# Kernel optimization log

Hardware: AMD Instinct MI355X
Metric: run time of the kernel (lower is better)

The kernel has to match this reference:

```python
import jax, jax.numpy as jnp
import numpy as np

# Dimensions (match init_kwargs / input_specs)
B, C, H, W = 16, 16, 64, 64
N = H * W          # num_nodes
D_E = 64           # node_embed_dim
D_H = 128          # gnn_hidden_dim
D_R = 256          # readout_output_dim


def _param(key, shape, fan_in):
    return jax.random.normal(key, shape, jnp.float32) * (1.0 / np.sqrt(fan_in))


def setup_inputs() -> dict:
    key = jax.random.key(0)
    ks = jax.random.split(key, 16)
    inp = {
        "obs": jax.random.normal(ks[0], (B, C, H, W), jnp.float32),
        # node_embedding MLP (2 layers: C -> D_E -> D_E)
        "e1_w": _param(ks[1], (C, D_E), C),   "e1_b": jnp.zeros((D_E,), jnp.float32),
        "e2_w": _param(ks[2], (D_E, D_E), D_E), "e2_b": jnp.zeros((D_E,), jnp.float32),
        # 3 GNN layers (Linear then adjacency aggregation)
        "g1_w": _param(ks[3], (D_E, D_H), D_E), "g1_b": jnp.zeros((D_H,), jnp.float32),
        "g2_w": _param(ks[4], (D_H, D_H), D_H), "g2_b": jnp.zeros((D_H,), jnp.float32),
        "g3_w": _param(ks[5], (D_H, D_H), D_H), "g3_b": jnp.zeros((D_H,), jnp.float32),
        # readout MLP (2 layers: D_H -> 2*D_H -> D_R)
        "r1_w": _param(ks[6], (D_H, 2 * D_H), D_H),   "r1_b": jnp.zeros((2 * D_H,), jnp.float32),
        "r2_w": _param(ks[7], (2 * D_H, D_R), 2 * D_H), "r2_b": jnp.zeros((D_R,), jnp.float32),
    }
    return inp


def _adj_norm():
    # 4-neighbor grid adjacency on an H x W grid, row-normalized (same for every
    # batch element, so build once as (N, N) instead of (B, N, N)).
    idx = jnp.arange(N)
    up = jnp.eye(N, k=-W, dtype=jnp.float32)                      # i > 0
    down = jnp.eye(N, k=W, dtype=jnp.float32)                     # i < H-1
    left = jnp.eye(N, k=-1, dtype=jnp.float32) * ((idx % W) != 0)[:, None]
    right = jnp.eye(N, k=1, dtype=jnp.float32) * ((idx % W) != (W - 1))[:, None]
    adj = up + down + left + right
    return adj / (adj.sum(axis=1, keepdims=True) + 1e-6)


def reference(obs, e1_w, e1_b, e2_w, e2_b,
              g1_w, g1_b, g2_w, g2_b, g3_w, g3_b,
              r1_w, r1_b, r2_w, r2_b):
    relu = jax.nn.relu
    # grid -> graph: (B, C, H, W) -> (B, N, C)
    x = jnp.transpose(obs, (0, 2, 3, 1)).reshape(B, N, C)
    # node embedding MLP (output activation per ding MLP default)
    h = relu(x @ e1_w + e1_b)
    h = relu(h @ e2_w + e2_b)
    A = _adj_norm()  # (N, N)
    for Wg, bg in ((g1_w, g1_b), (g2_w, g2_b), (g3_w, g3_b)):
        support = h @ Wg + bg                      # (B, N, D_H)
        h = relu(jnp.einsum('nm,bmf->bnf', A, support))
    g = h.mean(axis=1)                              # (B, D_H) graph readout
    g = relu(g @ r1_w + r1_b)
    return relu(g @ r2_w + r2_b)                    # (B, D_R)
```

## Files before the change

kernel.cpp:

```cpp
#include <hip/hip_runtime.h>


typedef __attribute__((ext_vector_type(8))) short bf16x8;
typedef __attribute__((ext_vector_type(4))) float f32x4;
#define MFMA(a, b, c) __builtin_amdgcn_mfma_f32_16x16x32_bf16(a, b, c, 0, 0, 0)

__device__ inline ushort bf16h(float x) {
    unsigned u = __float_as_uint(x);
    return (ushort)((u + 0x7fffu + ((u >> 16) & 1u)) >> 16);
}
__device__ inline void split_bf16(float x, ushort& hi, ushort& lo) {
    hi = bf16h(x);
    lo = bf16h(x - __uint_as_float(((unsigned)hi) << 16));
}
__device__ inline unsigned pack_split(float x) {
    unsigned u = __float_as_uint(x);
    unsigned hi = (u + 0x7fffu + ((u >> 16) & 1u)) >> 16;
    float r = x - __uint_as_float(hi << 16);
    unsigned v = __float_as_uint(r);
    unsigned lo = (v + 0x7fffu + ((v >> 16) & 1u)) >> 16;
    return (hi << 16) | lo;
}
__device__ inline void frag_packed(const unsigned* bp, bf16x8& bh, bf16x8& bl) {
    unsigned p[8];
#pragma unroll
    for (int j = 0; j < 8; j++) p[j] = bp[j * 65];
    union { bf16x8 v; unsigned d[4]; } H, L;
#pragma unroll
    for (int j = 0; j < 4; j++) {
        const unsigned e = p[2 * j], o = p[2 * j + 1];
        H.d[j] = (o & 0xFFFF0000u) | (e >> 16);
        L.d[j] = (o << 16) | (e & 0xFFFFu);
    }
    bh = H.v; bl = L.v;
}

__global__ void zero_kernel(float* __restrict__ p) {
    p[blockIdx.x * 256 + threadIdx.x] = 0.f;
}

__global__ __launch_bounds__(64) void wprep_kernel(
    const float* __restrict__ e1w, const float* __restrict__ e2w,
    const float* __restrict__ g1w, const float* __restrict__ g2w,
    const float* __restrict__ g3w, ushort* __restrict__ wf)
{
    const int blk = blockIdx.x, l = threadIdx.x;
    const float* src; int K, N, kc, t; ushort* dst;
    if (blk < 4)        { src = e1w; K = 16;  N = 64;  kc = 0; t = blk;      dst = wf; }
    else if (blk < 12)  { src = e2w; K = 64;  N = 64;  int u = blk - 4;  kc = u >> 2; t = u & 3; dst = wf + 4096; }
    else if (blk < 28)  { src = g1w; K = 64;  N = 128; int u = blk - 12; kc = u >> 3; t = u & 7; dst = wf + 12288; }
    else if (blk < 60)  { src = g2w; K = 128; N = 128; int u = blk - 28; kc = u >> 3; t = u & 7; dst = wf + 28672; }
    else                { src = g3w; K = 128; N = 128; int u = blk - 60; kc = u >> 3; t = u & 7; dst = wf + 61440; }
    const int T = (N == 64) ? 4 : 8;
    ushort* uh = dst + ((kc * T + t) * 2 + 0) * 512 + l * 8;
    ushort* ul = dst + ((kc * T + t) * 2 + 1) * 512 + l * 8;
    const int f = t * 16 + (l & 15);
    const int kb = kc * 32 + ((l >> 4) << 3);
#pragma unroll
    for (int j = 0; j < 8; j++) {
        const int k = kb + j;
        const float w = (k < K) ? src[k * N + f] : 0.f;
        ushort hi, lo; split_bf16(w, hi, lo);
        uh[j] = hi; ul[j] = lo;
    }
}

__global__ __launch_bounds__(256, 4) void embed_kernel(
    const float* __restrict__ obs, const ushort* __restrict__ wf,
    const float* __restrict__ e1b, const float* __restrict__ e2b,
    float* __restrict__ h0)
{
    __shared__ unsigned Xs[32 * 65];
    __shared__ unsigned Hs[64 * 65];
    const int tid = threadIdx.x, b = blockIdx.x >> 6, row = blockIdx.x & 63;
    const int lane = tid & 63, w = tid >> 6, quad = lane >> 4, nl = lane & 15;
    const int cp = tid >> 4, nq = tid & 15;

    const float4 x4 = *(const float4*)(obs + ((size_t)(b * 16 + cp) << 12) + row * 64 + nq * 4);
    unsigned* xp = Xs + cp * 65 + nq * 4;
    xp[0] = pack_split(x4.x); xp[1] = pack_split(x4.y);
    xp[2] = pack_split(x4.z); xp[3] = pack_split(x4.w);
    unsigned* zp = Xs + (16 + cp) * 65 + nq * 4;
    zp[0] = 0u; zp[1] = 0u; zp[2] = 0u; zp[3] = 0u;
    __syncthreads();

    {
        const ushort* wp = wf + lane * 8;
        const bf16x8 wh = *(const bf16x8*)(wp + (w * 2) * 512);
        const bf16x8 wl = *(const bf16x8*)(wp + (w * 2 + 1) * 512);
#pragma unroll
        for (int nt = 0; nt < 4; nt++) {
            const unsigned* bp = Xs + (quad * 8) * 65 + nt * 16 + nl;
            bf16x8 bh, bl; frag_packed(bp, bh, bl);
            f32x4 c = {0.f, 0.f, 0.f, 0.f};
            c = MFMA(wh, bh, c); c = MFMA(wh, bl, c); c = MFMA(wl, bh, c);
#pragma unroll
            for (int reg = 0; reg < 4; reg++) {
                const int fm = 16 * w + quad * 4 + reg;
                Hs[fm * 65 + nt * 16 + nl] = pack_split(fmaxf(c[reg] + e1b[fm], 0.f));
            }
        }
    }
    __syncthreads();

    const ushort* e2f = wf + 4096;
    f32x4 a2[4];
#pragma unroll
    for (int nt = 0; nt < 4; nt++) a2[nt] = (f32x4){0.f, 0.f, 0.f, 0.f};
#pragma unroll
    for (int kc = 0; kc < 2; kc++) {
        const ushort* wp = e2f + lane * 8;
        const bf16x8 wh = *(const bf16x8*)(wp + ((kc * 4 + w) * 2) * 512);
        const bf16x8 wl = *(const bf16x8*)(wp + ((kc * 4 + w) * 2 + 1) * 512);
#pragma unroll
        for (int nt = 0; nt < 4; nt++) {
            const unsigned* bp = Hs + (kc * 32 + quad * 8) * 65 + nt * 16 + nl;
            bf16x8 bh, bl; frag_packed(bp, bh, bl);
            a2[nt] = MFMA(wh, bh, a2[nt]);
            a2[nt] = MFMA(wh, bl, a2[nt]);
            a2[nt] = MFMA(wl, bh, a2[nt]);
        }
    }
#pragma unroll
    for (int reg = 0; reg < 4; reg++) {
        const int f = 16 * w + quad * 4 + reg;
        const float bv = e2b[f];
#pragma unroll
        for (int nt = 0; nt < 4; nt++)
            h0[((size_t)(b * 64 + f) << 12) + row * 64 + nt * 16 + nl] =
                fmaxf(a2[nt][reg] + bv, 0.f);
    }
}

template <int K, bool MEAN>
__global__ __launch_bounds__(256, 4) void gnn_kernel(
    const float* __restrict__ hin, const ushort* __restrict__ wf,
    const float* __restrict__ bias, float* __restrict__ hout,
    float* __restrict__ gsum)
{
    constexpr int NH = K / 64;
    __shared__ unsigned As[NH][64 * 65];
    const int tid = threadIdx.x;
    const int bid = ((blockIdx.x & 7) << 7) | (blockIdx.x >> 3);
    const int b = bid >> 6, row = bid & 63;
    const int lane = tid & 63, w = tid >> 6, quad = lane >> 4, nl = lane & 15;
    const int kp = tid >> 4, nq = tid & 15;
    const float* hb = hin + (size_t)b * K * 4096;
    const int rowu = (row > 0) ? row - 1 : row;
    const int rowd = (row < 63) ? row + 1 : row;
    const float su = (row > 0) ? 1.f : 0.f;
    const float sd = (row < 63) ? 1.f : 0.f;
    float inv[4];
#pragma unroll
    for (int i = 0; i < 4; i++) {
        const int n = nq * 4 + i;
        const int deg = (row > 0) + (row < 63) + (n > 0) + (n < 63);
        inv[i] = 1.f / ((float)deg + 1e-6f);
    }

    f32x4 acc[4][2];
#pragma unroll
    for (int nt = 0; nt < 4; nt++) {
        acc[nt][0] = (f32x4){0.f, 0.f, 0.f, 0.f};
        acc[nt][1] = (f32x4){0.f, 0.f, 0.f, 0.f};
    }

    float4 c4[4], u4[4], d4[4];
    auto load_half = [&](int kh) {
#pragma unroll
        for (int it = 0; it < 4; it++) {
            const int kk = it * 16 + kp;
            const float* pk = hb + ((size_t)(kh * 64 + kk) << 12) + nq * 4;
            c4[it] = *(const float4*)(pk + row * 64);
            u4[it] = *(const float4*)(pk + rowu * 64);
            d4[it] = *(const float4*)(pk + rowd * 64);
        }
    };
    auto stage = [&](int kh) {
        unsigned* dst = As[kh];
#pragma unroll
        for (int it = 0; it < 4; it++) {
            const int kk = it * 16 + kp;
            const float pw = __shfl_up(c4[it].w, 1);
            const float nx = __shfl_down(c4[it].x, 1);
            const float lx = (nq > 0) ? pw : 0.f;
            const float rw = (nq < 15) ? nx : 0.f;
            unsigned* ap = dst + kk * 65 + nq * 4;
            ap[0] = pack_split((su * u4[it].x + sd * d4[it].x + lx + c4[it].y) * inv[0]);
            ap[1] = pack_split((su * u4[it].y + sd * d4[it].y + c4[it].x + c4[it].z) * inv[1]);
            ap[2] = pack_split((su * u4[it].z + sd * d4[it].z + c4[it].y + c4[it].w) * inv[2]);
            ap[3] = pack_split((su * u4[it].w + sd * d4[it].w + c4[it].z + rw) * inv[3]);
        }
    };
    auto consume = [&](int kh) {
        const unsigned* src = As[kh];
#pragma unroll
        for (int kc = 0; kc < 2; kc++) {
            const int kcg = kh * 2 + kc;
            const ushort* wp = wf + lane * 8;
            const bf16x8 wh0 = *(const bf16x8*)(wp + ((kcg * 8 + 2 * w)     * 2)     * 512);
            const bf16x8 wl0 = *(const bf16x8*)(wp + ((kcg * 8 + 2 * w)     * 2 + 1) * 512);
            const bf16x8 wh1 = *(const bf16x8*)(wp + ((kcg * 8 + 2 * w + 1) * 2)     * 512);
            const bf16x8 wl1 = *(const bf16x8*)(wp + ((kcg * 8 + 2 * w + 1) * 2 + 1) * 512);
#pragma unroll
            for (int nt = 0; nt < 4; nt++) {
                const unsigned* bp = src + (kc * 32 + quad * 8) * 65 + nt * 16 + nl;
                bf16x8 bh, bl; frag_packed(bp, bh, bl);
                acc[nt][0] = MFMA(wh0, bh, acc[nt][0]);
                acc[nt][0] = MFMA(wh0, bl, acc[nt][0]);
                acc[nt][0] = MFMA(wl0, bh, acc[nt][0]);
                acc[nt][1] = MFMA(wh1, bh, acc[nt][1]);
                acc[nt][1] = MFMA(wh1, bl, acc[nt][1]);
                acc[nt][1] = MFMA(wl1, bh, acc[nt][1]);
            }
        }
    };

    load_half(0);
    stage(0);
    __syncthreads();
#pragma unroll
    for (int kh = 0; kh < NH; kh++) {
        if (kh + 1 < NH) load_half(kh + 1);
        consume(kh);
        if (kh + 1 < NH) {
            stage(kh + 1);
            __syncthreads();
        }
    }

    if (!MEAN) {
#pragma unroll
        for (int ftl = 0; ftl < 2; ftl++) {
            const int fb = 32 * w + 16 * ftl + quad * 4;
            const float b0 = bias[fb], b1 = bias[fb + 1], b2 = bias[fb + 2], b3 = bias[fb + 3];
#pragma unroll
            for (int nt = 0; nt < 4; nt++) {
                const int n = 16 * nt + nl;
                const int deg = (row > 0) + (row < 63) + (n > 0) + (n < 63);
                const float rs = (float)deg / ((float)deg + 1e-6f);
                float* op = hout + ((size_t)(b * 128 + fb) << 12) + row * 64 + n;
                op[0]        = fmaxf(acc[nt][ftl][0] + rs * b0, 0.f);
                op[1u << 12] = fmaxf(acc[nt][ftl][1] + rs * b1, 0.f);
                op[2u << 12] = fmaxf(acc[nt][ftl][2] + rs * b2, 0.f);
                op[3u << 12] = fmaxf(acc[nt][ftl][3] + rs * b3, 0.f);
            }
        }
    } else {
#pragma unroll
        for (int ftl = 0; ftl < 2; ftl++) {
            const int fb = 32 * w + 16 * ftl + quad * 4;
#pragma unroll
            for (int reg = 0; reg < 4; reg++) {
                const float bv = bias[fb + reg];
                float v = 0.f;
#pragma unroll
                for (int nt = 0; nt < 4; nt++) {
                    const int n = 16 * nt + nl;
                    const int deg = (row > 0) + (row < 63) + (n > 0) + (n < 63);
                    const float rs = (float)deg / ((float)deg + 1e-6f);
                    v += fmaxf(acc[nt][ftl][reg] + rs * bv, 0.f);
                }
                v += __shfl_xor(v, 1); v += __shfl_xor(v, 2);
                v += __shfl_xor(v, 4); v += __shfl_xor(v, 8);
                if (nl == 0) atomicAdd(&gsum[b * 128 + fb + reg], v * (1.f / 4096.f));
            }
        }
    }
}

__global__ __launch_bounds__(256) void readout_kernel(
    const float* __restrict__ gsum, const float* __restrict__ r1w,
    const float* __restrict__ r1b, const float* __restrict__ r2w,
    const float* __restrict__ r2b, float* __restrict__ out)
{
    __shared__ float gs[128];
    __shared__ float g2[256];
    const int b = blockIdx.x, tid = threadIdx.x;
    if (tid < 128) gs[tid] = gsum[b * 128 + tid];
    __syncthreads();
    float a = r1b[tid];
#pragma unroll 16
    for (int k = 0; k < 128; k++) a = fmaf(gs[k], r1w[k * 256 + tid], a);
    g2[tid] = fmaxf(a, 0.f);
    __syncthreads();
    float a2 = r2b[tid];
#pragma unroll 16
    for (int k = 0; k < 256; k++) a2 = fmaf(g2[k], r2w[k * 256 + tid], a2);
    out[b * 256 + tid] = fmaxf(a2, 0.f);
}

extern "C" void kernel_launch(void* const* d_in, const int* in_sizes, int n_in,
                              void* d_out, int out_size, void* d_ws, size_t ws_size,
                              hipStream_t stream)
{
    const float* obs = (const float*)d_in[0];
    const float* e1w = (const float*)d_in[1];
    const float* e1b = (const float*)d_in[2];
    const float* e2w = (const float*)d_in[3];
    const float* e2b = (const float*)d_in[4];
    const float* g1w = (const float*)d_in[5];
    const float* g1b = (const float*)d_in[6];
    const float* g2w = (const float*)d_in[7];
    const float* g2b = (const float*)d_in[8];
    const float* g3w = (const float*)d_in[9];
    const float* g3b = (const float*)d_in[10];
    const float* r1w = (const float*)d_in[11];
    const float* r1b = (const float*)d_in[12];
    const float* r2w = (const float*)d_in[13];
    const float* r2b = (const float*)d_in[14];
    float* out = (float*)d_out;
    float* ws = (float*)d_ws;

    float* h0 = ws;
    float* h1 = ws + 4194304;
    float* h2 = ws + 4194304 + 8388608;
    float* gsum = (float*)((char*)d_ws + 80u * 1024u * 1024u);
    ushort* wfb = (ushort*)((char*)d_ws + 80u * 1024u * 1024u + 8192u);

    hipLaunchKernelGGL(zero_kernel, dim3(8), dim3(256), 0, stream, gsum);
    hipLaunchKernelGGL(wprep_kernel, dim3(92), dim3(64), 0, stream,
                       e1w, e2w, g1w, g2w, g3w, wfb);
    hipLaunchKernelGGL(embed_kernel, dim3(1024), dim3(256), 0, stream,
                       obs, wfb, e1b, e2b, h0);
    hipLaunchKernelGGL((gnn_kernel<64, false>), dim3(1024), dim3(256), 0, stream,
                       h0, wfb + 12288, g1b, h1, nullptr);
    hipLaunchKernelGGL((gnn_kernel<128, false>), dim3(1024), dim3(256), 0, stream,
                       h1, wfb + 28672, g2b, h2, nullptr);
    hipLaunchKernelGGL((gnn_kernel<128, true>), dim3(1024), dim3(256), 0, stream,
                       h2, wfb + 61440, g3b, nullptr, gsum);
    hipLaunchKernelGGL(readout_kernel, dim3(16), dim3(256), 0, stream,
                       gsum, r1w, r1b, r2w, r2b, out);
}
```

Before: 165.8 us.

## Interleave neighbor loads with LDS staging, fold zeroing into weight prep

The GNN kernel now loads and stages each half of the input in groups of two, so staging one group overlaps the loads of the next and fewer float4 registers stay live. Staging of the next half now happens before the MFMA consume of the current half instead of after it. The low bf16 part in pack_split is truncated instead of rounded, and the gsum zeroing moves into extra blocks of the weight-prep kernel to save a launch. Moving the staging ahead of consume removes the overlap of global loads with MFMA work, and truncating the low part loses a little precision.

After: 163.1 us. About the same (-1.6%).

```diff
diff --git a/kernel.cpp b/kernel.cpp
--- a/kernel.cpp
+++ b/kernel.cpp
@@ -17,9 +17,7 @@
     unsigned u = __float_as_uint(x);
     unsigned hi = (u + 0x7fffu + ((u >> 16) & 1u)) >> 16;
     float r = x - __uint_as_float(hi << 16);
-    unsigned v = __float_as_uint(r);
-    unsigned lo = (v + 0x7fffu + ((v >> 16) & 1u)) >> 16;
-    return (hi << 16) | lo;
+    return (hi << 16) | (__float_as_uint(r) >> 16);
 }
 __device__ inline void frag_packed(const unsigned* bp, bf16x8& bh, bf16x8& bl) {
     unsigned p[8];
@@ -35,16 +33,17 @@
     bh = H.v; bl = L.v;
 }
 
-__global__ void zero_kernel(float* __restrict__ p) {
-    p[blockIdx.x * 256 + threadIdx.x] = 0.f;
-}
-
 __global__ __launch_bounds__(64) void wprep_kernel(
     const float* __restrict__ e1w, const float* __restrict__ e2w,
     const float* __restrict__ g1w, const float* __restrict__ g2w,
-    const float* __restrict__ g3w, ushort* __restrict__ wf)
+    const float* __restrict__ g3w, ushort* __restrict__ wf,
+    float* __restrict__ gsum)
 {
     const int blk = blockIdx.x, l = threadIdx.x;
+    if (blk >= 92) {
+        gsum[(blk - 92) * 64 + l] = 0.f;
+        return;
+    }
     const float* src; int K, N, kc, t; ushort* dst;
     if (blk < 4)        { src = e1w; K = 16;  N = 64;  kc = 0; t = blk;      dst = wf; }
     else if (blk < 12)  { src = e2w; K = 64;  N = 64;  int u = blk - 4;  kc = u >> 2; t = u & 3; dst = wf + 4096; }
@@ -165,32 +164,35 @@
         acc[nt][1] = (f32x4){0.f, 0.f, 0.f, 0.f};
     }
 
-    float4 c4[4], u4[4], d4[4];
-    auto load_half = [&](int kh) {
-#pragma unroll
-        for (int it = 0; it < 4; it++) {
-            const int kk = it * 16 + kp;
-            const float* pk = hb + ((size_t)(kh * 64 + kk) << 12) + nq * 4;
-            c4[it] = *(const float4*)(pk + row * 64);
-            u4[it] = *(const float4*)(pk + rowu * 64);
-            d4[it] = *(const float4*)(pk + rowd * 64);
-        }
+    auto load_group = [&](int kh, int it, float4& c, float4& u, float4& d) {
+        const int kk = it * 16 + kp;
+        const float* pk = hb + ((size_t)(kh * 64 + kk) << 12) + nq * 4;
+        c = *(const float4*)(pk + row * 64);
+        u = *(const float4*)(pk + rowu * 64);
+        d = *(const float4*)(pk + rowd * 64);
     };
-    auto stage = [&](int kh) {
-        unsigned* dst = As[kh];
-#pragma unroll
-        for (int it = 0; it < 4; it++) {
-            const int kk = it * 16 + kp;
-            const float pw = __shfl_up(c4[it].w, 1);
-            const float nx = __shfl_down(c4[it].x, 1);
-            const float lx = (nq > 0) ? pw : 0.f;
-            const float rw = (nq < 15) ? nx : 0.f;
-            unsigned* ap = dst + kk * 65 + nq * 4;
-            ap[0] = pack_split((su * u4[it].x + sd * d4[it].x + lx + c4[it].y) * inv[0]);
-            ap[1] = pack_split((su * u4[it].y + sd * d4[it].y + c4[it].x + c4[it].z) * inv[1]);
-            ap[2] = pack_split((su * u4[it].z + sd * d4[it].z + c4[it].y + c4[it].w) * inv[2]);
-            ap[3] = pack_split((su * u4[it].w + sd * d4[it].w + c4[it].z + rw) * inv[3]);
-        }
+    auto stage_group = [&](int kh, int it, const float4& c, const float4& u, const float4& d) {
+        const int kk = it * 16 + kp;
+        const float pw = __shfl_up(c.w, 1);
+        const float nx = __shfl_down(c.x, 1);
+        const float lx = (nq > 0) ? pw : 0.f;
+        const float rw = (nq < 15) ? nx : 0.f;
+        unsigned* ap = As[kh] + kk * 65 + nq * 4;
+        ap[0] = pack_split((su * u.x + sd * d.x + lx + c.y) * inv[0]);
+        ap[1] = pack_split((su * u.y + sd * d.y + c.x + c.z) * inv[1]);
+        ap[2] = pack_split((su * u.z + sd * d.z + c.y + c.w) * inv[2]);
+        ap[3] = pack_split((su * u.w + sd * d.w + c.z + rw) * inv[3]);
+    };
+    auto load_stage_half = [&](int kh) {
+        float4 c0, u0, d0, c1, u1, d1;
+        load_group(kh, 0, c0, u0, d0);
+        load_group(kh, 1, c1, u1, d1);
+        stage_group(kh, 0, c0, u0, d0);
+        load_group(kh, 2, c0, u0, d0);
+        stage_group(kh, 1, c1, u1, d1);
+        load_group(kh, 3, c1, u1, d1);
+        stage_group(kh, 2, c0, u0, d0);
+        stage_group(kh, 3, c1, u1, d1);
     };
     auto consume = [&](int kh) {
         const unsigned* src = As[kh];
@@ -216,17 +218,13 @@
         }
     };
 
-    load_half(0);
-    stage(0);
+    load_stage_half(0);
     __syncthreads();
 #pragma unroll
     for (int kh = 0; kh < NH; kh++) {
-        if (kh + 1 < NH) load_half(kh + 1);
+        if (kh + 1 < NH) load_stage_half(kh + 1);
         consume(kh);
-        if (kh + 1 < NH) {
-            stage(kh + 1);
-            __syncthreads();
-        }
+        if (kh + 1 < NH) __syncthreads();
     }
 
     if (!MEAN) {
@@ -318,9 +316,8 @@
     float* gsum = (float*)((char*)d_ws + 80u * 1024u * 1024u);
     ushort* wfb = (ushort*)((char*)d_ws + 80u * 1024u * 1024u + 8192u);
 
-    hipLaunchKernelGGL(zero_kernel, dim3(8), dim3(256), 0, stream, gsum);
-    hipLaunchKernelGGL(wprep_kernel, dim3(92), dim3(64), 0, stream,
-                       e1w, e2w, g1w, g2w, g3w, wfb);
+    hipLaunchKernelGGL(wprep_kernel, dim3(124), dim3(64), 0, stream,
+                       e1w, e2w, g1w, g2w, g3w, wfb, gsum);
     hipLaunchKernelGGL(embed_kernel, dim3(1024), dim3(256), 0, stream,
                        obs, wfb, e1b, e2b, h0);
     hipLaunchKernelGGL((gnn_kernel<64, false>), dim3(1024), dim3(256), 0, stream,
```
